# Optimization experiments

Hardware: AMD Instinct MI355X
Metric: run time of the kernel (lower is better)

## Reference

```python
import jax, jax.numpy as jnp
import numpy as np

# NFFT config (matches torch NFFT(N=(256,256), m=4, sigma=2.0))
N = (256, 256)          # output Fourier grid
n = (512, 512)          # oversampled grid (2*(int(sigma*N)//2))
m = 4                   # window half-width -> (2m)^2 = 64 taps per point
B, C, M = 2, 2, 200000  # batch, channels, nonuniform points
SIGMA = tuple(n[i] / N[i] for i in range(2))  # KaiserBesselWindow sigma = n/N


def kb_phi(k):
    """Kaiser-Bessel window phi(k), k: (..., 2). Matches KaiserBesselWindow.forward."""
    nv = jnp.asarray(n, dtype=k.dtype)
    b = (2.0 - 1.0 / jnp.asarray(SIGMA, dtype=k.dtype)) * jnp.pi
    t = m * m - (nv * k) ** 2
    safe = t > 0
    arg = jnp.sqrt(jnp.where(safe, t, 1.0))
    out = jnp.where(safe, jnp.sinh(b * arg) / (arg * jnp.pi), 0.0)  # nan_to_num(...,0) equiv.
    return jnp.prod(out, axis=-1)


def kb_phi_hat():
    """Fourier coefficients of the window on the N-grid (KaiserBesselWindow.ft)."""
    grids = jnp.meshgrid(*[jnp.arange(-(N[i] // 2), N[i] // 2, dtype=jnp.float32)
                           for i in range(2)], indexing='ij')
    inds = jnp.stack(grids, axis=-1)                                 # (N1,N2,2)
    nv = jnp.asarray(n, jnp.float32)
    b = (2.0 - 1.0 / jnp.asarray(SIGMA, jnp.float32)) * jnp.pi
    ft = jnp.i0(m * jnp.sqrt(b ** 2 - (2.0 * jnp.pi * inds / nv) ** 2))
    return jnp.prod(ft, axis=-1)                                     # (N1,N2)


def setup_inputs() -> dict:
    key = jax.random.key(0)
    k1, k2, k3 = jax.random.split(key, 3)
    x = jax.random.uniform(k1, (B, 1, M, 2), dtype=jnp.float32) - 0.5  # points in [-1/2,1/2)
    f_hat_real = jax.random.normal(k2, (B, C, N[0], N[1]), dtype=jnp.float32)
    f_hat_imag = jax.random.normal(k3, (B, C, N[0], N[1]), dtype=jnp.float32)
    return {"x": x, "f_hat_real": f_hat_real, "f_hat_imag": f_hat_imag}


def reference(x, f_hat_real, f_hat_imag):
    f_hat = f_hat_real + 1j * f_hat_imag                              # (B,C,N1,N2) complex64
    # deconvolve by window Fourier coefficients
    g_hat = f_hat / kb_phi_hat()
    # zero-pad to oversampled grid n
    cut = [(n[i] - N[i]) // 2 for i in range(2)]
    g_hat = jnp.pad(g_hat, ((0, 0), (0, 0), (cut[0], cut[0]), (cut[1], cut[1])))
    ax = (-2, -1)
    g = jnp.fft.ifftshift(jnp.fft.fft2(jnp.fft.fftshift(g_hat, ax), norm='backward'), ax)
    # windowed gather (sparse_convolution): (2m)^2 taps per nonuniform point
    r = jnp.arange(2 * m, dtype=jnp.int32)
    off = jnp.stack(jnp.meshgrid(r, r, indexing='ij'), axis=-1).reshape(-1, 2)  # (64,2)
    nv = jnp.asarray(n, jnp.float32)
    base = jnp.ceil(x * nv).astype(jnp.int32) - m                     # (B,1,M,2)
    inds = base[None] + off[:, None, None, None, :]                   # (64,B,1,M,2)
    w = kb_phi(x[None] - inds.astype(jnp.float32) / nv)               # (64,B,1,M)
    half = jnp.asarray([n[0] // 2, n[1] // 2], jnp.int32)
    nn = jnp.asarray(n, jnp.int32)
    im = (inds + half) % nn                                           # wrap onto grid
    g2 = jnp.transpose(g, (0, 2, 3, 1))                               # (B,n1,n2,C)
    bidx = jnp.arange(B, dtype=jnp.int32)[None, :, None, None]
    gl = g2[bidx, im[..., 0], im[..., 1]]                             # (64,B,1,M,C)
    f = jnp.sum(gl * w[..., None].astype(gl.dtype), axis=0)           # (B,1,M,C)
    return jnp.transpose(f[:, 0], (0, 2, 1))                          # (B,C,M) complex64
```

## Files before the change

### kernel.cpp

```cpp
#include <hip/hip_runtime.h>
#include <math.h>


#define NGRID 512
#define NSMALL 256
#define MW 4
#define BB 2
#define CC 2
#define MPTS 200000
#define PLANE (BB * CC * MPTS)
#define LPAD4 513
#define IMG4 (NGRID * NGRID)
#define G16OFF(b) ((size_t)(b) * 524288 + 131072)

__device__ __forceinline__ float nfft29781_i0_large(float z) {
    float inv = __builtin_amdgcn_rcpf(z);
    float p = 1.0f + inv * (0.125f + inv * (0.0703125f
              + inv * (0.0732421875f + inv * 0.112152099609375f)));
    return __expf(z) * rsqrtf(2.0f * (float)M_PI * z) * p;
}

__device__ __forceinline__ int nfft29781_brev9(int v) {
    return (int)(__brev((unsigned)v) >> 23);
}

__device__ __forceinline__ unsigned nfft29781_bf16pack(float a, float b) {
    unsigned ua = __float_as_uint(a);
    ua += 0x7FFFu + ((ua >> 16) & 1u);
    unsigned ub = __float_as_uint(b);
    ub += 0x7FFFu + ((ub >> 16) & 1u);
    return (ua >> 16) | (ub & 0xFFFF0000u);
}

__global__ __launch_bounds__(256) void nfft29781_rows2(const float* __restrict__ fr,
                                                       const float* __restrict__ fi,
                                                       float4* __restrict__ G32) {
    __shared__ float4 s[NGRID];
    int tid = threadIdx.x;
    int b   = blockIdx.x >> 8;
    int a1  = blockIdx.x & 255;

    const float bcon  = 1.5f * (float)M_PI;
    const float scale = 2.0f * (float)M_PI / (float)NGRID;
    float k1 = (float)(a1 - 128) * scale;
    float p1 = nfft29781_i0_large((float)MW * sqrtf(bcon * bcon - k1 * k1));

    int a2 = tid ^ 128;
    float k2 = (float)(a2 - 128) * scale;
    float p2 = nfft29781_i0_large((float)MW * sqrtf(bcon * bcon - k2 * k2));
    float invp = __builtin_amdgcn_rcpf(p1 * p2);

    size_t s0 = ((size_t)(b * CC + 0) * NSMALL + a1) * NSMALL + a2;
    size_t s1 = ((size_t)(b * CC + 1) * NSMALL + a1) * NSMALL + a2;
    float4 v = make_float4(fr[s0] * invp, fi[s0] * invp,
                           fr[s1] * invp, fi[s1] * invp);

    int j2v = (tid < 128) ? tid : tid + 256;
    int pidx = nfft29781_brev9(j2v);
    int pe = pidx & ~1;
    s[pe]     = v;
    s[pe + 1] = (pidx & 1) ? make_float4(-v.x, -v.y, -v.z, -v.w) : v;
    __syncthreads();

    #pragma unroll
    for (int st = 1; st < 9; ++st) {
        int half = 1 << st;
        int pos = tid & (half - 1);
        int i0 = ((tid >> st) << (st + 1)) + pos;
        int i1 = i0 + half;
        float sn, cs;
        if (st == 1) {
            cs = pos ? 0.0f : 1.0f;
            sn = pos ? -1.0f : 0.0f;
        } else {
            float ang = -(float)M_PI * (float)pos / (float)half;
            __sincosf(ang, &sn, &cs);
        }
        float4 a = s[i0];
        float4 bq = s[i1];
        float4 tw;
        tw.x = bq.x * cs - bq.y * sn;  tw.y = bq.x * sn + bq.y * cs;
        tw.z = bq.z * cs - bq.w * sn;  tw.w = bq.z * sn + bq.w * cs;
        s[i0] = make_float4(a.x + tw.x, a.y + tw.y, a.z + tw.z, a.w + tw.w);
        s[i1] = make_float4(a.x - tw.x, a.y - tw.y, a.z - tw.z, a.w - tw.w);
        __syncthreads();
    }

    int j1 = (a1 < 128) ? a1 + 384 : a1 - 128;
    float4* Gb = G32 + (size_t)b * IMG4 + (size_t)j1 * NGRID;
    Gb[tid]       = s[tid];
    Gb[tid + 256] = s[tid + 256];
}

__global__ __launch_bounds__(256) void nfft29781_cols2(float4* __restrict__ G32) {
    __shared__ float4 s[4 * LPAD4];
    int tid  = threadIdx.x;
    int b    = blockIdx.x >> 7;
    int col0 = (blockIdx.x & 127) << 2;
    const float4* Gb = G32 + (size_t)b * IMG4;

    #pragma unroll
    for (int it = 0; it < 4; ++it) {
        int e  = it * 256 + tid;
        int cp = e & 3;
        int q  = e >> 2;
        int r  = (q < 128) ? q : q + 256;
        float4 v = Gb[(size_t)r * NGRID + col0 + cp];
        int pidx = nfft29781_brev9(r);
        int pe = pidx & ~1;
        float4* scw = s + cp * LPAD4;
        scw[pe]     = v;
        scw[pe + 1] = (pidx & 1) ? make_float4(-v.x, -v.y, -v.z, -v.w) : v;
    }
    __syncthreads();

    int c = tid & 3;
    int w = tid >> 2;
    float4* sc = s + c * LPAD4;
    #pragma unroll
    for (int st = 1; st < 9; ++st) {
        const int half = 1 << st;
        float csk[4], snk[4];
        if (st <= 6) {
            int pos = w & (half - 1);
            float sn, cs;
            if (st == 1) {
                cs = pos ? 0.0f : 1.0f;
                sn = pos ? -1.0f : 0.0f;
            } else {
                float ang = -(float)M_PI * (float)pos / (float)half;
                __sincosf(ang, &sn, &cs);
            }
            csk[0] = csk[1] = csk[2] = csk[3] = cs;
            snk[0] = snk[1] = snk[2] = snk[3] = sn;
        } else if (st == 7) {
            #pragma unroll
            for (int k = 0; k < 2; ++k) {
                int pos = (w + (k << 6)) & 127;
                float ang = -(float)M_PI * (float)pos / 128.0f;
                __sincosf(ang, &snk[k], &csk[k]);
            }
            csk[2] = csk[0]; snk[2] = snk[0];
            csk[3] = csk[1]; snk[3] = snk[1];
        } else {
            #pragma unroll
            for (int k = 0; k < 4; ++k) {
                int pos = w + (k << 6);
                float ang = -(float)M_PI * (float)pos / 256.0f;
                __sincosf(ang, &snk[k], &csk[k]);
            }
        }
        #pragma unroll
        for (int k = 0; k < 4; ++k) {
            int bf  = w + (k << 6);
            int pos = bf & (half - 1);
            int i0  = ((bf >> st) << (st + 1)) + pos;
            int i1  = i0 + half;
            float cs = csk[k], sn = snk[k];
            float4 a = sc[i0];
            float4 bb = sc[i1];
            float4 tw;
            tw.x = bb.x * cs - bb.y * sn;  tw.y = bb.x * sn + bb.y * cs;
            tw.z = bb.z * cs - bb.w * sn;  tw.w = bb.z * sn + bb.w * cs;
            sc[i0] = make_float4(a.x + tw.x, a.y + tw.y, a.z + tw.z, a.w + tw.w);
            sc[i1] = make_float4(a.x - tw.x, a.y - tw.y, a.z - tw.z, a.w - tw.w);
        }
        __syncthreads();
    }

    uint2* G16 = (uint2*)G32 + G16OFF(b);
    #pragma unroll
    for (int it = 0; it < 8; ++it) {
        int e  = it * 256 + tid;
        int cp = e & 3;
        int r  = e >> 2;
        float4 v = s[cp * LPAD4 + r];
        uint2 pk;
        pk.x = nfft29781_bf16pack(v.x, v.y);
        pk.y = nfft29781_bf16pack(v.z, v.w);
        G16[(size_t)r * NGRID + col0 + cp] = pk;
    }
}

__global__ __launch_bounds__(256) void nfft29781_gather_bf16(const float* __restrict__ x,
                                                             const uint2* __restrict__ G16base,
                                                             float* __restrict__ out,
                                                             int out_elems) {
    int t  = blockIdx.x * blockDim.x + threadIdx.x;
    int j  = t & 7;
    int pp = t >> 3;
    if (pp >= BB * MPTS) return;
    int b  = (pp >= MPTS) ? 1 : 0;
    int pt = pp - b * MPTS;

    float u0 = x[(size_t)pp * 2 + 0] * (float)NGRID;
    float u1 = x[(size_t)pp * 2 + 1] * (float)NGRID;

    float c0 = ceilf(u0), c1 = ceilf(u1);
    int base0 = (int)c0 - MW;
    int base1 = (int)c1 - MW;
    float d0 = c0 - u0, d1 = c1 - u1;

    const float bw = 1.5f * (float)M_PI;
    const float invpi = 1.0f / (float)M_PI;
    float w0m, w1m;
    {
        float nk = (float)(MW - j) - d0;
        float tt = (float)(MW * MW) - nk * nk;
        w0m = 0.0f;
        if (tt > 0.0f) {
            float ra = __builtin_amdgcn_rsqf(tt);
            float a  = tt * ra;
            float e  = __expf(bw * a);
            w0m = (e - __builtin_amdgcn_rcpf(e)) * (0.5f * invpi) * ra;
        }
        nk = (float)(MW - j) - d1;
        tt = (float)(MW * MW) - nk * nk;
        w1m = 0.0f;
        if (tt > 0.0f) {
            float ra = __builtin_amdgcn_rsqf(tt);
            float a  = tt * ra;
            float e  = __expf(bw * a);
            w1m = (e - __builtin_amdgcn_rcpf(e)) * (0.5f * invpi) * ra;
        }
    }

    const uint2* Gi = G16base + G16OFF(b);
    int cix = (base1 + j) & (NGRID - 1);
    int lanebase = (threadIdx.x & 63) & ~7;

    float a0x = 0.0f, a0y = 0.0f, a1x = 0.0f, a1y = 0.0f;
    #pragma unroll
    for (int i = 0; i < 8; ++i) {
        float w0i = __shfl(w0m, lanebase + i, 64);
        uint2 g = Gi[(size_t)(((base0 + i) & (NGRID - 1)) << 9) + cix];
        float g0x = __uint_as_float(g.x << 16);
        float g0y = __uint_as_float(g.x & 0xFFFF0000u);
        float g1x = __uint_as_float(g.y << 16);
        float g1y = __uint_as_float(g.y & 0xFFFF0000u);
        a0x += w0i * g0x;  a0y += w0i * g0y;
        a1x += w0i * g1x;  a1y += w0i * g1y;
    }
    a0x *= w1m;  a0y *= w1m;  a1x *= w1m;  a1y *= w1m;

    #pragma unroll
    for (int msk = 1; msk < 8; msk <<= 1) {
        a0x += __shfl_xor(a0x, msk, 64);
        a0y += __shfl_xor(a0y, msk, 64);
        a1x += __shfl_xor(a1x, msk, 64);
        a1y += __shfl_xor(a1y, msk, 64);
    }

    if (j == 0) {
        size_t o0 = (size_t)(b * CC) * MPTS + pt;
        size_t o1 = o0 + MPTS;
        if (o0 < (size_t)out_elems)         out[o0]         = a0x;
        if (PLANE + o0 < (size_t)out_elems) out[PLANE + o0] = a0y;
        if (o1 < (size_t)out_elems)         out[o1]         = a1x;
        if (PLANE + o1 < (size_t)out_elems) out[PLANE + o1] = a1y;
    }
}

extern "C" void kernel_launch(void* const* d_in, const int* in_sizes, int n_in,
                              void* d_out, int out_size, void* d_ws, size_t ws_size,
                              hipStream_t stream) {
    (void)in_sizes; (void)n_in;
    const float* x  = (const float*)d_in[0];
    const float* fr = (const float*)d_in[1];
    const float* fi = (const float*)d_in[2];
    float*  out = (float*)d_out;
    float4* G32 = (float4*)d_ws;

    const size_t fullBytes = (size_t)BB * IMG4 * sizeof(float4);
    if (ws_size < fullBytes) return;

    nfft29781_rows2<<<BB * NSMALL, 256, 0, stream>>>(fr, fi, G32);
    nfft29781_cols2<<<BB * (NGRID / 4), 256, 0, stream>>>(G32);
    int gthreads = BB * MPTS * 8;
    nfft29781_gather_bf16<<<(gthreads + 255) / 256, 256, 0, stream>>>(
        x, (const uint2*)d_ws, out, out_size);
}
```

Before: 95.05 us.

## Use radix-4 FFT stages and halve gather threads per point

Row and column FFTs now run four radix-4 passes instead of eight radix-2 passes. This halves the number of shared-memory round trips and barriers, and derives the first twiddle from the second by squaring. The gather kernel now uses 4 lanes per nonuniform point instead of 8. Each lane handles two columns and computes both halves of the row weights, which cuts shuffle-reduction steps and thread count. In exchange each lane holds more registers and issues two loads per row, and the squared twiddles add a little extra rounding error.

```diff
diff --git a/kernel.cpp b/kernel.cpp
--- a/kernel.cpp
+++ b/kernel.cpp
@@ -32,6 +32,49 @@
     return (ua >> 16) | (ub & 0xFFFF0000u);
 }
 
+__device__ __forceinline__ float4 nfft29781_cmul4(float4 v, float cs, float sn) {
+    return make_float4(v.x * cs - v.y * sn, v.x * sn + v.y * cs,
+                       v.z * cs - v.w * sn, v.z * sn + v.w * cs);
+}
+__device__ __forceinline__ float4 nfft29781_add4(float4 a, float4 b) {
+    return make_float4(a.x + b.x, a.y + b.y, a.z + b.z, a.w + b.w);
+}
+__device__ __forceinline__ float4 nfft29781_sub4(float4 a, float4 b) {
+    return make_float4(a.x - b.x, a.y - b.y, a.z - b.z, a.w - b.w);
+}
+__device__ __forceinline__ float4 nfft29781_mnegi4(float4 v) {
+    return make_float4(v.y, -v.x, v.w, -v.z);
+}
+
+__device__ __forceinline__ void nfft29781_r4(float4* p, int i0, int L,
+                                             float cs2, float sn2) {
+    float cs1 = cs2 * cs2 - sn2 * sn2;
+    float sn1 = 2.0f * cs2 * sn2;
+    float4 a0 = p[i0], a1 = p[i0 + L], a2 = p[i0 + 2 * L], a3 = p[i0 + 3 * L];
+    float4 t1 = nfft29781_cmul4(a1, cs1, sn1);
+    float4 t3 = nfft29781_cmul4(a3, cs1, sn1);
+    float4 u0 = nfft29781_add4(a0, t1);
+    float4 u1 = nfft29781_sub4(a0, t1);
+    float4 u2 = nfft29781_add4(a2, t3);
+    float4 u3 = nfft29781_sub4(a2, t3);
+    float4 v2 = nfft29781_cmul4(u2, cs2, sn2);
+    float4 v3 = nfft29781_mnegi4(nfft29781_cmul4(u3, cs2, sn2));
+    p[i0]         = nfft29781_add4(u0, v2);
+    p[i0 + L]     = nfft29781_add4(u1, v3);
+    p[i0 + 2 * L] = nfft29781_sub4(u0, v2);
+    p[i0 + 3 * L] = nfft29781_sub4(u1, v3);
+}
+
+__device__ __forceinline__ void nfft29781_tw(int pos, int L, float* cs2, float* sn2) {
+    if (L == 2) {
+        *cs2 = pos ? 0.70710678118f : 1.0f;
+        *sn2 = pos ? -0.70710678118f : 0.0f;
+    } else {
+        float ang = (-(float)M_PI / (float)(2 * L)) * (float)pos;
+        __sincosf(ang, sn2, cs2);
+    }
+}
+
 __global__ __launch_bounds__(256) void nfft29781_rows2(const float* __restrict__ fr,
                                                        const float* __restrict__ fi,
                                                        float4* __restrict__ G32) {
@@ -63,26 +106,17 @@
     __syncthreads();
 
     #pragma unroll
-    for (int st = 1; st < 9; ++st) {
-        int half = 1 << st;
-        int pos = tid & (half - 1);
-        int i0 = ((tid >> st) << (st + 1)) + pos;
-        int i1 = i0 + half;
-        float sn, cs;
-        if (st == 1) {
-            cs = pos ? 0.0f : 1.0f;
-            sn = pos ? -1.0f : 0.0f;
-        } else {
-            float ang = -(float)M_PI * (float)pos / (float)half;
-            __sincosf(ang, &sn, &cs);
+    for (int si = 0; si < 4; ++si) {
+        const int st = 1 + 2 * si;
+        const int L  = 1 << st;
+        if (tid < 128) {
+            int g   = tid;
+            int pos = g & (L - 1);
+            int i0  = ((g >> st) << (st + 2)) + pos;
+            float cs2, sn2;
+            nfft29781_tw(pos, L, &cs2, &sn2);
+            nfft29781_r4(s, i0, L, cs2, sn2);
         }
-        float4 a = s[i0];
-        float4 bq = s[i1];
-        float4 tw;
-        tw.x = bq.x * cs - bq.y * sn;  tw.y = bq.x * sn + bq.y * cs;
-        tw.z = bq.z * cs - bq.w * sn;  tw.w = bq.z * sn + bq.w * cs;
-        s[i0] = make_float4(a.x + tw.x, a.y + tw.y, a.z + tw.z, a.w + tw.w);
-        s[i1] = make_float4(a.x - tw.x, a.y - tw.y, a.z - tw.z, a.w - tw.w);
         __syncthreads();
     }
 
@@ -118,52 +152,17 @@
     int w = tid >> 2;
     float4* sc = s + c * LPAD4;
     #pragma unroll
-    for (int st = 1; st < 9; ++st) {
-        const int half = 1 << st;
-        float csk[4], snk[4];
-        if (st <= 6) {
-            int pos = w & (half - 1);
-            float sn, cs;
-            if (st == 1) {
-                cs = pos ? 0.0f : 1.0f;
-                sn = pos ? -1.0f : 0.0f;
-            } else {
-                float ang = -(float)M_PI * (float)pos / (float)half;
-                __sincosf(ang, &sn, &cs);
-            }
-            csk[0] = csk[1] = csk[2] = csk[3] = cs;
-            snk[0] = snk[1] = snk[2] = snk[3] = sn;
-        } else if (st == 7) {
-            #pragma unroll
-            for (int k = 0; k < 2; ++k) {
-                int pos = (w + (k << 6)) & 127;
-                float ang = -(float)M_PI * (float)pos / 128.0f;
-                __sincosf(ang, &snk[k], &csk[k]);
-            }
-            csk[2] = csk[0]; snk[2] = snk[0];
-            csk[3] = csk[1]; snk[3] = snk[1];
-        } else {
-            #pragma unroll
-            for (int k = 0; k < 4; ++k) {
-                int pos = w + (k << 6);
-                float ang = -(float)M_PI * (float)pos / 256.0f;
-                __sincosf(ang, &snk[k], &csk[k]);
-            }
-        }
+    for (int si = 0; si < 4; ++si) {
+        const int st = 1 + 2 * si;
+        const int L  = 1 << st;
         #pragma unroll
-        for (int k = 0; k < 4; ++k) {
-            int bf  = w + (k << 6);
-            int pos = bf & (half - 1);
-            int i0  = ((bf >> st) << (st + 1)) + pos;
-            int i1  = i0 + half;
-            float cs = csk[k], sn = snk[k];
-            float4 a = sc[i0];
-            float4 bb = sc[i1];
-            float4 tw;
-            tw.x = bb.x * cs - bb.y * sn;  tw.y = bb.x * sn + bb.y * cs;
-            tw.z = bb.z * cs - bb.w * sn;  tw.w = bb.z * sn + bb.w * cs;
-            sc[i0] = make_float4(a.x + tw.x, a.y + tw.y, a.z + tw.z, a.w + tw.w);
-            sc[i1] = make_float4(a.x - tw.x, a.y - tw.y, a.z - tw.z, a.w - tw.w);
+        for (int k = 0; k < 2; ++k) {
+            int g   = w + (k << 6);
+            int pos = g & (L - 1);
+            int i0  = ((g >> st) << (st + 2)) + pos;
+            float cs2, sn2;
+            nfft29781_tw(pos, L, &cs2, &sn2);
+            nfft29781_r4(sc, i0, L, cs2, sn2);
         }
         __syncthreads();
     }
@@ -182,13 +181,22 @@
     }
 }
 
+__device__ __forceinline__ float nfft29781_kbw(float nk) {
+    float tt = (float)(MW * MW) - nk * nk;
+    if (tt <= 0.0f) return 0.0f;
+    float ra = __builtin_amdgcn_rsqf(tt);
+    float a  = tt * ra;
+    float e  = __expf(1.5f * (float)M_PI * a);
+    return (e - __builtin_amdgcn_rcpf(e)) * (0.5f / (float)M_PI) * ra;
+}
+
 __global__ __launch_bounds__(256) void nfft29781_gather_bf16(const float* __restrict__ x,
                                                              const uint2* __restrict__ G16base,
                                                              float* __restrict__ out,
                                                              int out_elems) {
     int t  = blockIdx.x * blockDim.x + threadIdx.x;
-    int j  = t & 7;
-    int pp = t >> 3;
+    int j  = t & 3;
+    int pp = t >> 2;
     if (pp >= BB * MPTS) return;
     int b  = (pp >= MPTS) ? 1 : 0;
     int pt = pp - b * MPTS;
@@ -201,50 +209,41 @@
     int base1 = (int)c1 - MW;
     float d0 = c0 - u0, d1 = c1 - u1;
 
-    const float bw = 1.5f * (float)M_PI;
-    const float invpi = 1.0f / (float)M_PI;
-    float w0m, w1m;
-    {
-        float nk = (float)(MW - j) - d0;
-        float tt = (float)(MW * MW) - nk * nk;
-        w0m = 0.0f;
-        if (tt > 0.0f) {
-            float ra = __builtin_amdgcn_rsqf(tt);
-            float a  = tt * ra;
-            float e  = __expf(bw * a);
-            w0m = (e - __builtin_amdgcn_rcpf(e)) * (0.5f * invpi) * ra;
-        }
-        nk = (float)(MW - j) - d1;
-        tt = (float)(MW * MW) - nk * nk;
-        w1m = 0.0f;
-        if (tt > 0.0f) {
-            float ra = __builtin_amdgcn_rsqf(tt);
-            float a  = tt * ra;
-            float e  = __expf(bw * a);
-            w1m = (e - __builtin_amdgcn_rcpf(e)) * (0.5f * invpi) * ra;
-        }
-    }
+    float w0a = nfft29781_kbw((float)(MW - j) - d0);
+    float w0b = nfft29781_kbw((float)(MW - j - 4) - d0);
+    float w1a = nfft29781_kbw((float)(MW - 2 * j) - d1);
+    float w1b = nfft29781_kbw((float)(MW - 2 * j - 1) - d1);
 
     const uint2* Gi = G16base + G16OFF(b);
-    int cix = (base1 + j) & (NGRID - 1);
-    int lanebase = (threadIdx.x & 63) & ~7;
-
-    float a0x = 0.0f, a0y = 0.0f, a1x = 0.0f, a1y = 0.0f;
+    int cixA = (base1 + 2 * j) & (NGRID - 1);
+    int cixB = (base1 + 2 * j + 1) & (NGRID - 1);
+    int lanebase = (threadIdx.x & 63) & ~3;
+
+    float sA0 = 0.0f, sA1 = 0.0f, sA2 = 0.0f, sA3 = 0.0f;
+    float sB0 = 0.0f, sB1 = 0.0f, sB2 = 0.0f, sB3 = 0.0f;
     #pragma unroll
     for (int i = 0; i < 8; ++i) {
-        float w0i = __shfl(w0m, lanebase + i, 64);
-        uint2 g = Gi[(size_t)(((base0 + i) & (NGRID - 1)) << 9) + cix];
-        float g0x = __uint_as_float(g.x << 16);
-        float g0y = __uint_as_float(g.x & 0xFFFF0000u);
-        float g1x = __uint_as_float(g.y << 16);
-        float g1y = __uint_as_float(g.y & 0xFFFF0000u);
-        a0x += w0i * g0x;  a0y += w0i * g0y;
-        a1x += w0i * g1x;  a1y += w0i * g1y;
-    }
-    a0x *= w1m;  a0y *= w1m;  a1x *= w1m;  a1y *= w1m;
-
-    #pragma unroll
-    for (int msk = 1; msk < 8; msk <<= 1) {
+        float w0i = (i < 4) ? __shfl(w0a, lanebase + i, 64)
+                            : __shfl(w0b, lanebase + (i - 4), 64);
+        size_t rb = (size_t)(((base0 + i) & (NGRID - 1)) << 9);
+        uint2 gA = Gi[rb + cixA];
+        uint2 gB = Gi[rb + cixB];
+        sA0 += w0i * __uint_as_float(gA.x << 16);
+        sA1 += w0i * __uint_as_float(gA.x & 0xFFFF0000u);
+        sA2 += w0i * __uint_as_float(gA.y << 16);
+        sA3 += w0i * __uint_as_float(gA.y & 0xFFFF0000u);
+        sB0 += w0i * __uint_as_float(gB.x << 16);
+        sB1 += w0i * __uint_as_float(gB.x & 0xFFFF0000u);
+        sB2 += w0i * __uint_as_float(gB.y << 16);
+        sB3 += w0i * __uint_as_float(gB.y & 0xFFFF0000u);
+    }
+    float a0x = sA0 * w1a + sB0 * w1b;
+    float a0y = sA1 * w1a + sB1 * w1b;
+    float a1x = sA2 * w1a + sB2 * w1b;
+    float a1y = sA3 * w1a + sB3 * w1b;
+
+    #pragma unroll
+    for (int msk = 1; msk < 4; msk <<= 1) {
         a0x += __shfl_xor(a0x, msk, 64);
         a0y += __shfl_xor(a0y, msk, 64);
         a1x += __shfl_xor(a1x, msk, 64);
@@ -276,7 +275,7 @@
 
     nfft29781_rows2<<<BB * NSMALL, 256, 0, stream>>>(fr, fi, G32);
     nfft29781_cols2<<<BB * (NGRID / 4), 256, 0, stream>>>(G32);
-    int gthreads = BB * MPTS * 8;
+    int gthreads = BB * MPTS * 4;
     nfft29781_gather_bf16<<<(gthreads + 255) / 256, 256, 0, stream>>>(
         x, (const uint2*)d_ws, out, out_size);
 }
```

After: 97.49 us. 2.6% more time.

## Fuse row and column FFT kernels with a software grid barrier

Applied to the files above, without the earlier changes.

Merges the row-FFT and column-FFT kernels into one persistent kernel of 512 blocks. A global atomic counter barrier sits between the two phases, and each block in the column phase now handles 2 columns instead of 4. The goal is to remove one kernel launch and its inter-kernel gap. In exchange it depends on all 512 blocks being co-resident, otherwise the barrier deadlocks, and it adds spin-wait cost.

```diff
diff --git a/kernel.cpp b/kernel.cpp
--- a/kernel.cpp
+++ b/kernel.cpp
@@ -11,7 +11,10 @@
 #define PLANE (BB * CC * MPTS)
 #define LPAD4 513
 #define IMG4 (NGRID * NGRID)
+#define NBLK 512
 #define G16OFF(b) ((size_t)(b) * 524288 + 131072)
+
+__device__ unsigned nfft29781_bar = 0;
 
 __device__ __forceinline__ float nfft29781_i0_large(float z) {
     float inv = __builtin_amdgcn_rcpf(z);
@@ -32,97 +35,44 @@
     return (ua >> 16) | (ub & 0xFFFF0000u);
 }
 
-__global__ __launch_bounds__(256) void nfft29781_rows2(const float* __restrict__ fr,
+__global__ __launch_bounds__(256) void nfft29781_fft2d(const float* __restrict__ fr,
                                                        const float* __restrict__ fi,
                                                        float4* __restrict__ G32) {
-    __shared__ float4 s[NGRID];
+    __shared__ float4 s[2 * LPAD4];
     int tid = threadIdx.x;
-    int b   = blockIdx.x >> 8;
-    int a1  = blockIdx.x & 255;
-
-    const float bcon  = 1.5f * (float)M_PI;
-    const float scale = 2.0f * (float)M_PI / (float)NGRID;
-    float k1 = (float)(a1 - 128) * scale;
-    float p1 = nfft29781_i0_large((float)MW * sqrtf(bcon * bcon - k1 * k1));
-
-    int a2 = tid ^ 128;
-    float k2 = (float)(a2 - 128) * scale;
-    float p2 = nfft29781_i0_large((float)MW * sqrtf(bcon * bcon - k2 * k2));
-    float invp = __builtin_amdgcn_rcpf(p1 * p2);
-
-    size_t s0 = ((size_t)(b * CC + 0) * NSMALL + a1) * NSMALL + a2;
-    size_t s1 = ((size_t)(b * CC + 1) * NSMALL + a1) * NSMALL + a2;
-    float4 v = make_float4(fr[s0] * invp, fi[s0] * invp,
-                           fr[s1] * invp, fi[s1] * invp);
-
-    int j2v = (tid < 128) ? tid : tid + 256;
-    int pidx = nfft29781_brev9(j2v);
-    int pe = pidx & ~1;
-    s[pe]     = v;
-    s[pe + 1] = (pidx & 1) ? make_float4(-v.x, -v.y, -v.z, -v.w) : v;
-    __syncthreads();
-
-    #pragma unroll
-    for (int st = 1; st < 9; ++st) {
-        int half = 1 << st;
-        int pos = tid & (half - 1);
-        int i0 = ((tid >> st) << (st + 1)) + pos;
-        int i1 = i0 + half;
-        float sn, cs;
-        if (st == 1) {
-            cs = pos ? 0.0f : 1.0f;
-            sn = pos ? -1.0f : 0.0f;
-        } else {
-            float ang = -(float)M_PI * (float)pos / (float)half;
-            __sincosf(ang, &sn, &cs);
-        }
-        float4 a = s[i0];
-        float4 bq = s[i1];
-        float4 tw;
-        tw.x = bq.x * cs - bq.y * sn;  tw.y = bq.x * sn + bq.y * cs;
-        tw.z = bq.z * cs - bq.w * sn;  tw.w = bq.z * sn + bq.w * cs;
-        s[i0] = make_float4(a.x + tw.x, a.y + tw.y, a.z + tw.z, a.w + tw.w);
-        s[i1] = make_float4(a.x - tw.x, a.y - tw.y, a.z - tw.z, a.w - tw.w);
+
+    {
+        int b   = blockIdx.x >> 8;
+        int a1  = blockIdx.x & 255;
+
+        const float bcon  = 1.5f * (float)M_PI;
+        const float scale = 2.0f * (float)M_PI / (float)NGRID;
+        float k1 = (float)(a1 - 128) * scale;
+        float p1 = nfft29781_i0_large((float)MW * sqrtf(bcon * bcon - k1 * k1));
+
+        int a2 = tid ^ 128;
+        float k2 = (float)(a2 - 128) * scale;
+        float p2 = nfft29781_i0_large((float)MW * sqrtf(bcon * bcon - k2 * k2));
+        float invp = __builtin_amdgcn_rcpf(p1 * p2);
+
+        size_t s0 = ((size_t)(b * CC + 0) * NSMALL + a1) * NSMALL + a2;
+        size_t s1 = ((size_t)(b * CC + 1) * NSMALL + a1) * NSMALL + a2;
+        float4 v = make_float4(fr[s0] * invp, fi[s0] * invp,
+                               fr[s1] * invp, fi[s1] * invp);
+
+        int j2v = (tid < 128) ? tid : tid + 256;
+        int pidx = nfft29781_brev9(j2v);
+        int pe = pidx & ~1;
+        s[pe]     = v;
+        s[pe + 1] = (pidx & 1) ? make_float4(-v.x, -v.y, -v.z, -v.w) : v;
         __syncthreads();
-    }
-
-    int j1 = (a1 < 128) ? a1 + 384 : a1 - 128;
-    float4* Gb = G32 + (size_t)b * IMG4 + (size_t)j1 * NGRID;
-    Gb[tid]       = s[tid];
-    Gb[tid + 256] = s[tid + 256];
-}
-
-__global__ __launch_bounds__(256) void nfft29781_cols2(float4* __restrict__ G32) {
-    __shared__ float4 s[4 * LPAD4];
-    int tid  = threadIdx.x;
-    int b    = blockIdx.x >> 7;
-    int col0 = (blockIdx.x & 127) << 2;
-    const float4* Gb = G32 + (size_t)b * IMG4;
-
-    #pragma unroll
-    for (int it = 0; it < 4; ++it) {
-        int e  = it * 256 + tid;
-        int cp = e & 3;
-        int q  = e >> 2;
-        int r  = (q < 128) ? q : q + 256;
-        float4 v = Gb[(size_t)r * NGRID + col0 + cp];
-        int pidx = nfft29781_brev9(r);
-        int pe = pidx & ~1;
-        float4* scw = s + cp * LPAD4;
-        scw[pe]     = v;
-        scw[pe + 1] = (pidx & 1) ? make_float4(-v.x, -v.y, -v.z, -v.w) : v;
-    }
-    __syncthreads();
-
-    int c = tid & 3;
-    int w = tid >> 2;
-    float4* sc = s + c * LPAD4;
-    #pragma unroll
-    for (int st = 1; st < 9; ++st) {
-        const int half = 1 << st;
-        float csk[4], snk[4];
-        if (st <= 6) {
-            int pos = w & (half - 1);
+
+        #pragma unroll
+        for (int st = 1; st < 9; ++st) {
+            int half = 1 << st;
+            int pos = tid & (half - 1);
+            int i0 = ((tid >> st) << (st + 1)) + pos;
+            int i1 = i0 + half;
             float sn, cs;
             if (st == 1) {
                 cs = pos ? 0.0f : 1.0f;
@@ -131,54 +81,109 @@
                 float ang = -(float)M_PI * (float)pos / (float)half;
                 __sincosf(ang, &sn, &cs);
             }
-            csk[0] = csk[1] = csk[2] = csk[3] = cs;
-            snk[0] = snk[1] = snk[2] = snk[3] = sn;
-        } else if (st == 7) {
+            float4 a = s[i0];
+            float4 bq = s[i1];
+            float4 tw;
+            tw.x = bq.x * cs - bq.y * sn;  tw.y = bq.x * sn + bq.y * cs;
+            tw.z = bq.z * cs - bq.w * sn;  tw.w = bq.z * sn + bq.w * cs;
+            s[i0] = make_float4(a.x + tw.x, a.y + tw.y, a.z + tw.z, a.w + tw.w);
+            s[i1] = make_float4(a.x - tw.x, a.y - tw.y, a.z - tw.z, a.w - tw.w);
+            __syncthreads();
+        }
+
+        int j1 = (a1 < 128) ? a1 + 384 : a1 - 128;
+        float4* Gb = G32 + (size_t)b * IMG4 + (size_t)j1 * NGRID;
+        Gb[tid]       = s[tid];
+        Gb[tid + 256] = s[tid + 256];
+    }
+
+    __syncthreads();
+    if (tid == 0) {
+        __threadfence();
+        unsigned old = __hip_atomic_fetch_add(&nfft29781_bar, 1u,
+                           __ATOMIC_ACQ_REL, __HIP_MEMORY_SCOPE_AGENT);
+        unsigned target = (old / (unsigned)NBLK + 1u) * (unsigned)NBLK;
+        while (__hip_atomic_load(&nfft29781_bar, __ATOMIC_RELAXED,
+                                 __HIP_MEMORY_SCOPE_AGENT) < target) {
+            __builtin_amdgcn_s_sleep(1);
+        }
+        __threadfence();
+    }
+    __syncthreads();
+
+    {
+        int b    = blockIdx.x >> 8;
+        int col0 = (blockIdx.x & 255) << 1;
+        const float4* Gb = G32 + (size_t)b * IMG4;
+
+        #pragma unroll
+        for (int it = 0; it < 2; ++it) {
+            int e  = it * 256 + tid;
+            int cp = e & 1;
+            int q  = e >> 1;
+            int r  = (q < 128) ? q : q + 256;
+            float4 v = Gb[(size_t)r * NGRID + col0 + cp];
+            int pidx = nfft29781_brev9(r);
+            int pe = pidx & ~1;
+            float4* scw = s + cp * LPAD4;
+            scw[pe]     = v;
+            scw[pe + 1] = (pidx & 1) ? make_float4(-v.x, -v.y, -v.z, -v.w) : v;
+        }
+        __syncthreads();
+
+        int c = tid & 1;
+        int w = tid >> 1;
+        float4* sc = s + c * LPAD4;
+        #pragma unroll
+        for (int st = 1; st < 9; ++st) {
+            const int half = 1 << st;
+            float csk[2], snk[2];
+            if (st == 1) {
+                int pos = w & 1;
+                csk[0] = pos ? 0.0f : 1.0f;
+                snk[0] = pos ? -1.0f : 0.0f;
+                csk[1] = csk[0]; snk[1] = snk[0];
+            } else if (st < 8) {
+                int pos = w & (half - 1);
+                float ang = -(float)M_PI * (float)pos / (float)half;
+                __sincosf(ang, &snk[0], &csk[0]);
+                csk[1] = csk[0]; snk[1] = snk[0];
+            } else {
+                float ang0 = -(float)M_PI * (float)w / 256.0f;
+                __sincosf(ang0, &snk[0], &csk[0]);
+                float ang1 = -(float)M_PI * (float)(w + 128) / 256.0f;
+                __sincosf(ang1, &snk[1], &csk[1]);
+            }
             #pragma unroll
             for (int k = 0; k < 2; ++k) {
-                int pos = (w + (k << 6)) & 127;
-                float ang = -(float)M_PI * (float)pos / 128.0f;
-                __sincosf(ang, &snk[k], &csk[k]);
+                int bf  = w + (k << 7);
+                int pos = bf & (half - 1);
+                int i0  = ((bf >> st) << (st + 1)) + pos;
+                int i1  = i0 + half;
+                float cs = csk[k], sn = snk[k];
+                float4 a = sc[i0];
+                float4 bb = sc[i1];
+                float4 tw;
+                tw.x = bb.x * cs - bb.y * sn;  tw.y = bb.x * sn + bb.y * cs;
+                tw.z = bb.z * cs - bb.w * sn;  tw.w = bb.z * sn + bb.w * cs;
+                sc[i0] = make_float4(a.x + tw.x, a.y + tw.y, a.z + tw.z, a.w + tw.w);
+                sc[i1] = make_float4(a.x - tw.x, a.y - tw.y, a.z - tw.z, a.w - tw.w);
             }
-            csk[2] = csk[0]; snk[2] = snk[0];
-            csk[3] = csk[1]; snk[3] = snk[1];
-        } else {
-            #pragma unroll
-            for (int k = 0; k < 4; ++k) {
-                int pos = w + (k << 6);
-                float ang = -(float)M_PI * (float)pos / 256.0f;
-                __sincosf(ang, &snk[k], &csk[k]);
-            }
-        }
-        #pragma unroll
-        for (int k = 0; k < 4; ++k) {
-            int bf  = w + (k << 6);
-            int pos = bf & (half - 1);
-            int i0  = ((bf >> st) << (st + 1)) + pos;
-            int i1  = i0 + half;
-            float cs = csk[k], sn = snk[k];
-            float4 a = sc[i0];
-            float4 bb = sc[i1];
-            float4 tw;
-            tw.x = bb.x * cs - bb.y * sn;  tw.y = bb.x * sn + bb.y * cs;
-            tw.z = bb.z * cs - bb.w * sn;  tw.w = bb.z * sn + bb.w * cs;
-            sc[i0] = make_float4(a.x + tw.x, a.y + tw.y, a.z + tw.z, a.w + tw.w);
-            sc[i1] = make_float4(a.x - tw.x, a.y - tw.y, a.z - tw.z, a.w - tw.w);
-        }
-        __syncthreads();
-    }
-
-    uint2* G16 = (uint2*)G32 + G16OFF(b);
-    #pragma unroll
-    for (int it = 0; it < 8; ++it) {
-        int e  = it * 256 + tid;
-        int cp = e & 3;
-        int r  = e >> 2;
-        float4 v = s[cp * LPAD4 + r];
-        uint2 pk;
-        pk.x = nfft29781_bf16pack(v.x, v.y);
-        pk.y = nfft29781_bf16pack(v.z, v.w);
-        G16[(size_t)r * NGRID + col0 + cp] = pk;
+            __syncthreads();
+        }
+
+        uint2* G16 = (uint2*)G32 + G16OFF(b);
+        #pragma unroll
+        for (int it = 0; it < 4; ++it) {
+            int e  = it * 256 + tid;
+            int cp = e & 1;
+            int r  = e >> 1;
+            float4 v = s[cp * LPAD4 + r];
+            uint2 pk;
+            pk.x = nfft29781_bf16pack(v.x, v.y);
+            pk.y = nfft29781_bf16pack(v.z, v.w);
+            G16[(size_t)r * NGRID + col0 + cp] = pk;
+        }
     }
 }
 
@@ -274,8 +279,7 @@
     const size_t fullBytes = (size_t)BB * IMG4 * sizeof(float4);
     if (ws_size < fullBytes) return;
 
-    nfft29781_rows2<<<BB * NSMALL, 256, 0, stream>>>(fr, fi, G32);
-    nfft29781_cols2<<<BB * (NGRID / 4), 256, 0, stream>>>(G32);
+    nfft29781_fft2d<<<NBLK, 256, 0, stream>>>(fr, fi, G32);
     int gthreads = BB * MPTS * 8;
     nfft29781_gather_bf16<<<(gthreads + 255) / 256, 256, 0, stream>>>(
         x, (const uint2*)d_ws, out, out_size);
```

Result: slower. 142.1 us (+49.5%).
